# Performance work log

Hardware: AMD Instinct MI355X
Metric: run time of the kernel (lower is better)

## Reference

```python
import jax, jax.numpy as jnp
import numpy as np

NUM_CLASSES = 128
COST_CLS = 2.0
COST_BBOX = 0.25
ALPHA = 0.25
GAMMA = 2.0
BBOX_NORM = np.array([1.0, 1.0, 1.0, 0.1, 0.1, 0.1, 1.0, 1.0, 0.1, 0.1], dtype=np.float32)


def _lsa(cost):
    # Jonker-Volgenant style shortest augmenting path Hungarian (e-maxx formulation).
    # cost: (n, m) float64 with n <= m. Returns col4row: for each row i, assigned column.
    n, m = cost.shape
    INF = 1e18
    a = np.zeros((n + 1, m + 1))
    a[1:, 1:] = cost
    u = np.zeros(n + 1)
    v = np.zeros(m + 1)
    p = np.zeros(m + 1, dtype=np.int64)   # p[j]: row (1-indexed) assigned to col j
    way = np.zeros(m + 1, dtype=np.int64)
    cols = np.arange(1, m + 1)
    for i in range(1, n + 1):
        p[0] = i
        j0 = 0
        minv = np.full(m + 1, INF)
        used = np.zeros(m + 1, dtype=bool)
        while True:
            used[j0] = True
            i0 = p[j0]
            cur = a[i0, 1:] - u[i0] - v[1:]
            better = (~used[1:]) & (cur < minv[1:])
            jb = cols[better]
            minv[jb] = cur[better]
            way[jb] = j0
            free = cols[~used[1:]]
            j1 = free[np.argmin(minv[free])]
            delta = minv[j1]
            uj = np.flatnonzero(used)
            u[p[uj]] += delta
            v[uj] -= delta
            nj = np.flatnonzero(~used)
            minv[nj] -= delta
            j0 = int(j1)
            if p[j0] == 0:
                break
        while j0:
            j1 = way[j0]
            p[j0] = p[j1]
            j0 = j1
    col4row = np.zeros(n, dtype=np.int64)
    for j in range(1, m + 1):
        if p[j]:
            col4row[p[j] - 1] = j - 1
    return col4row


def _match(cls_scores, bbox_preds, gt_labels, gt_bboxes):
    # Matching is done under no_grad in the original; host-side numpy mirrors scipy lsa.
    cs = np.asarray(cls_scores, np.float64)
    bp = np.asarray(bbox_preds, np.float64)
    gl = np.asarray(gt_labels)
    gb = np.asarray(gt_bboxes, np.float64)
    B = cs.shape[0]
    norm = BBOX_NORM.astype(np.float64)
    pred_idx = np.zeros(gl.shape, dtype=np.int64)
    for b in range(B):
        prob = 1.0 / (1.0 + np.exp(-np.clip(cs[b], -20.0, 20.0)))
        cost_cls = -prob[:, gl[b]]                                   # (Q, G)
        pn = np.clip(bp[b] / norm, -100, 100)
        gn = np.clip(gb[b] / norm, -100, 100)
        cost_bbox = np.abs(pn[:, None, :] - gn[None, :, :]).sum(-1)  # (Q, G) L1 cdist
        C = COST_CLS * cost_cls + COST_BBOX * cost_bbox
        pred_idx[b] = _lsa(C.T)   # for each gt g, its matched query index
    return pred_idx


def setup_inputs() -> dict:
    key = jax.random.key(0)
    k1, k2, k3, k4 = jax.random.split(key, 4)
    B, Q, G, C = 64, 2048, 64, NUM_CLASSES
    return {
        "cls_scores": jax.random.normal(k1, (B, Q, C), jnp.float32),
        "bbox_preds": jax.random.normal(k2, (B, Q, 10), jnp.float32),
        "gt_labels": jax.random.randint(k3, (B, G), 0, C),
        "gt_bboxes": jax.random.normal(k4, (B, G, 10), jnp.float32),
    }


def reference(cls_scores, bbox_preds, gt_labels, gt_bboxes):
    pred_idx = jnp.asarray(_match(cls_scores, bbox_preds, gt_labels, gt_bboxes))  # [B, G]
    B, Q, C = cls_scores.shape
    G = gt_labels.shape[1]
    b_idx = jnp.arange(B)[:, None]
    # one-hot classification targets at matched (query, label) positions
    onehot = jnp.zeros((B, Q, C), cls_scores.dtype).at[b_idx, pred_idx, gt_labels].set(1.0)
    prob = jax.nn.sigmoid(cls_scores)
    ce = -(onehot * jax.nn.log_sigmoid(cls_scores)
           + (1.0 - onehot) * jax.nn.log_sigmoid(-cls_scores))
    p_t = prob * onehot + (1.0 - prob) * (1.0 - onehot)
    focal_w = (ALPHA * onehot + (1.0 - ALPHA) * (1.0 - onehot)) * (1.0 - p_t) ** GAMMA
    loss_cls = (ce * focal_w).sum() / (G * B)   # per-batch sum / num_gt, then mean over B
    norm = jnp.asarray(BBOX_NORM)
    mp = bbox_preds[b_idx, pred_idx]            # [B, G, 10] matched predictions
    mg = gt_bboxes                              # gt_indices == arange(G): every gt matched
    loss_bbox = jnp.abs(mp / norm - mg / norm).mean()
    ml = cls_scores[b_idx, pred_idx]
    pos_acc = (jnp.argmax(ml, -1) == gt_labels).astype(jnp.float32).mean()
    xyz_err = jnp.abs(mp[..., :3] - mg[..., :3]).mean()
    matched = jnp.float32(G)
    return jnp.stack([loss_cls, loss_bbox, matched, pos_acc, xyz_err])
```

## Files before the change

### kernel.cpp

```cpp
#include <hip/hip_runtime.h>
#include <math.h>

#define NB 64
#define NQ 2048
#define NG 64
#define NC 128
#define TPB 256

#define WS_NEG   0
#define WS_POS   16384
#define WS_PRED  147456
#define WS_COST  163840
#define WS_NEED  (163840 + (size_t)NB * NG * NQ * 4)

__device__ __forceinline__ float normd(int d) {
    return (d == 3 || d == 4 || d == 5 || d == 8 || d == 9) ? 0.1f : 1.0f;
}
__device__ __forceinline__ float softplus_f(float x) {
    return x > 0.f ? x + log1pf(expf(-x)) : log1pf(expf(x));
}
__device__ __forceinline__ double neg_term(float x) {
    float s = 1.f / (1.f + expf(-x));
    return (double)(0.75f * s * s * softplus_f(x));
}
__device__ __forceinline__ double pos_term(float x) {
    float s = 1.f / (1.f + expf(-x));
    float om = 1.f - s;
    return (double)(0.25f * om * om * softplus_f(-x));
}
__device__ __forceinline__ float neg_term_fast(float x) {
    const float m = fmaxf(x, 0.f);
    const float a = __expf(x - m);
    const float bq = __expf(-m);
    const float den = a + bq;
    const float s = __fdividef(a, den);
    const float sp = m + __logf(den);
    return 0.75f * s * s * sp;
}

__device__ __forceinline__ unsigned dpp_min6(unsigned key) {
    unsigned t;
    t = (unsigned)__builtin_amdgcn_update_dpp((int)key, (int)key, 0x111, 0xF, 0xF, false);
    key = t < key ? t : key;
    t = (unsigned)__builtin_amdgcn_update_dpp((int)key, (int)key, 0x112, 0xF, 0xF, false);
    key = t < key ? t : key;
    t = (unsigned)__builtin_amdgcn_update_dpp((int)key, (int)key, 0x114, 0xF, 0xF, false);
    key = t < key ? t : key;
    t = (unsigned)__builtin_amdgcn_update_dpp((int)key, (int)key, 0x118, 0xF, 0xF, false);
    key = t < key ? t : key;
    t = (unsigned)__builtin_amdgcn_update_dpp((int)key, (int)key, 0x142, 0xF, 0xF, false);
    key = t < key ? t : key;
    t = (unsigned)__builtin_amdgcn_update_dpp((int)key, (int)key, 0x143, 0xF, 0xF, false);
    key = t < key ? t : key;
    return key;
}

__global__ __launch_bounds__(TPB) void cost_neg_kernel(
    const float* __restrict__ cls, const float* __restrict__ bp,
    const int* __restrict__ gl, const float* __restrict__ gb,
    float* __restrict__ C, double* __restrict__ negP)
{
    const int b = blockIdx.x >> 5;
    const int q0 = (blockIdx.x & 31) << 6;
    const int tid = threadIdx.x;
    __shared__ float cls_s[64 * 129];
    __shared__ float pn_s[10 * 64];
    __shared__ float gn_s[64 * 10];
    __shared__ int lbl_s[64];

    double negsum = 0.0;
    const float* clsb = cls + ((size_t)b * NQ + q0) * NC;
    for (int idx = tid; idx < 64 * 128; idx += TPB) {
        const int q = idx >> 7, c = idx & 127;
        const float x = clsb[idx];
        cls_s[q * 129 + c] = x;
        negsum += (double)neg_term_fast(x);
    }
    const float* bpb = bp + ((size_t)b * NQ + q0) * 10;
    for (int idx = tid; idx < 640; idx += TPB) {
        const int q = idx / 10, d = idx % 10;
        const float val = bpb[idx] / normd(d);
        pn_s[d * 64 + q] = fminf(100.f, fmaxf(-100.f, val));
    }
    const float* gbb = gb + (size_t)b * NG * 10;
    for (int idx = tid; idx < 640; idx += TPB) {
        const int g = idx / 10, d = idx % 10;
        const float val = gbb[idx] / normd(d);
        gn_s[g * 10 + d] = fminf(100.f, fmaxf(-100.f, val));
    }
    if (tid < NG) lbl_s[tid] = gl[b * NG + tid];
    __syncthreads();

    const int q = tid & 63;
    float pnq[10];
    #pragma unroll
    for (int d = 0; d < 10; ++d) pnq[d] = pn_s[d * 64 + q];
    for (int g = tid >> 6; g < NG; g += 4) {
        const int lbl = lbl_s[g];
        float x = cls_s[q * 129 + lbl];
        x = fminf(20.f, fmaxf(-20.f, x));
        const float s = __fdividef(1.f, 1.f + __expf(-x));
        float cb = 0.f;
        #pragma unroll
        for (int d = 0; d < 10; ++d) cb += fabsf(pnq[d] - gn_s[g * 10 + d]);
        C[((size_t)(b * NG + g)) * NQ + q0 + q] = -2.f * s + 0.25f * cb;
    }

    #pragma unroll
    for (int off = 32; off; off >>= 1) negsum += __shfl_down(negsum, off);
    __shared__ double bsum[4];
    if ((tid & 63) == 0) bsum[tid >> 6] = negsum;
    __syncthreads();
    if (tid == 0) negP[blockIdx.x] = bsum[0] + bsum[1] + bsum[2] + bsum[3];
}

__global__ __launch_bounds__(64, 1) void hungarian5_kernel(
    const float* __restrict__ C, int* __restrict__ pred)
{
    const int b = blockIdx.x;
    const int lane = threadIdx.x;
    __shared__ float u[NG + 1];
    __shared__ float usedD[NQ + 1];
    __shared__ int p[NQ + 1];
    __shared__ int way32[NQ + 1];

    for (int j = lane; j <= NQ; j += 64) { p[j] = 0; way32[j] = 0; }
    if (lane <= NG) u[lane] = 0.f;
    __syncthreads();

    const float* Cb = C + (size_t)b * NG * NQ;
    const int qbase = lane << 5;

    float vv[32];
    #pragma unroll
    for (int k = 0; k < 32; ++k) vv[k] = -16.f;
    unsigned amask = 0;

    float4 nx[8];
    {
        const float* r0 = Cb + qbase;
        #pragma unroll
        for (int m = 0; m < 8; ++m) nx[m] = reinterpret_cast<const float4*>(r0)[m];
    }

    for (int i = 1; i <= NG; ++i) {
        float madj[32];
        unsigned um = 0;

        unsigned m0 = 0xFFFFFFFFu, m1 = 0xFFFFFFFFu, m2 = 0xFFFFFFFFu, m3 = 0xFFFFFFFFu;
        #pragma unroll
        for (int m = 0; m < 8; ++m) {
            const float d0 = nx[m].x - vv[4*m+0];
            const float d1 = nx[m].y - vv[4*m+1];
            const float d2 = nx[m].z - vv[4*m+2];
            const float d3 = nx[m].w - vv[4*m+3];
            madj[4*m+0] = d0; madj[4*m+1] = d1; madj[4*m+2] = d2; madj[4*m+3] = d3;
            const unsigned k0 = (__float_as_uint(d0) & 0xFFFFF800u) | (unsigned)(qbase + 4*m+0);
            const unsigned k1 = (__float_as_uint(d1) & 0xFFFFF800u) | (unsigned)(qbase + 4*m+1);
            const unsigned k2 = (__float_as_uint(d2) & 0xFFFFF800u) | (unsigned)(qbase + 4*m+2);
            const unsigned k3 = (__float_as_uint(d3) & 0xFFFFF800u) | (unsigned)(qbase + 4*m+3);
            m0 = k0 < m0 ? k0 : m0;  m1 = k1 < m1 ? k1 : m1;
            m2 = k2 < m2 ? k2 : m2;  m3 = k3 < m3 ? k3 : m3;
        }
        if (i < NG) {
            const float* rn = Cb + (size_t)i * NQ + qbase;
            #pragma unroll
            for (int m = 0; m < 8; ++m) nx[m] = reinterpret_cast<const float4*>(rn)[m];
        }
        const unsigned ma = m0 < m1 ? m0 : m1;
        const unsigned mb = m2 < m3 ? m2 : m3;
        unsigned gkey = (unsigned)__builtin_amdgcn_readlane(
                            (int)dpp_min6(ma < mb ? ma : mb), 63);
        int q1 = (int)(gkey & 2047u);
        float D = __uint_as_float(gkey & 0xFFFFF800u);
        int ow = q1 >> 5, kk = q1 & 31;
        unsigned am_ow = (unsigned)__builtin_amdgcn_readlane((int)amask, ow);
        const bool assigned0 = (am_ow >> kk) & 1u;

        if (!assigned0) {
            if (lane == 0) { u[i] += D; p[q1 + 1] = i; }
        } else {
            if (lane == ow) { um |= 1u << kk; usedD[q1 + 1] = D; }
            #pragma unroll
            for (int k = 0; k < 32; ++k)
                if (k == kk && lane == ow) madj[k] = 1e30f;
            int j0 = q1 + 1;
            int i0 = p[j0];
            while (true) {
                const float s = u[i0] - D;
                const float* rr = Cb + (size_t)(i0 - 1) * NQ + qbase;
                float4 t[8];
                #pragma unroll
                for (int m = 0; m < 8; ++m) t[m] = reinterpret_cast<const float4*>(rr)[m];
                unsigned bk = 0xFFFFFFFFu;
                #pragma unroll
                for (int m = 0; m < 8; ++m) {
                    const float c[4] = {t[m].x, t[m].y, t[m].z, t[m].w};
                    #pragma unroll
                    for (int d = 0; d < 4; ++d) {
                        const int k = 4*m + d;
                        const float cand = c[d] - vv[k] - s;
                        if (!((um >> k) & 1u) && cand < madj[k]) {
                            madj[k] = cand;
                            way32[qbase + k + 1] = (i << 16) | j0;
                        }
                        const unsigned kb = (__float_as_uint(madj[k]) & 0xFFFFF800u)
                                          | (unsigned)(qbase + k);
                        bk = kb < bk ? kb : bk;
                    }
                }
                gkey = (unsigned)__builtin_amdgcn_readlane((int)dpp_min6(bk), 63);
                q1 = (int)(gkey & 2047u);
                D = __uint_as_float(gkey & 0xFFFFF800u);
                ow = q1 >> 5; kk = q1 & 31;
                am_ow = (unsigned)__builtin_amdgcn_readlane((int)amask, ow);
                if (!((am_ow >> kk) & 1u)) break;
                if (lane == ow) { um |= 1u << kk; usedD[q1 + 1] = D; }
                #pragma unroll
                for (int k = 0; k < 32; ++k)
                    if (k == kk && lane == ow) madj[k] = 1e30f;
                j0 = q1 + 1;
                i0 = p[j0];
            }
            #pragma unroll
            for (int k = 0; k < 32; ++k) {
                if ((um >> k) & 1u) {
                    const int j = qbase + k + 1;
                    const float dd = D - usedD[j];
                    vv[k] -= dd;
                    u[p[j]] += dd;
                }
            }
            if (lane == 0) {
                u[i] += D;
                int j = q1 + 1;
                while (true) {
                    const int w = way32[j];
                    const int par = ((w >> 16) == i) ? (w & 0xFFFF) : 0;
                    p[j] = par ? p[par] : i;
                    if (!par) break;
                    j = par;
                }
            }
        }
        if (lane == ow) amask |= 1u << kk;
    }

    for (int j = lane + 1; j <= NQ; j += 64) {
        const int pi = p[j];
        if (pi > 0) pred[b * NG + pi - 1] = j - 1;
    }
}

__global__ __launch_bounds__(TPB) void hungarian_fb_kernel(
    const float* __restrict__ cls, const float* __restrict__ bp,
    const int* __restrict__ gl, const float* __restrict__ gb,
    int* __restrict__ pred)
{
    const int b = blockIdx.x;
    const int tid = threadIdx.x;
    __shared__ float pn[10][NQ];
    __shared__ float gn[NG][10];
    __shared__ int lbls[NG];
    __shared__ double u[NG + 1];
    __shared__ double v[NQ + 1];
    __shared__ double minv[NQ + 1];
    __shared__ int p[NQ + 1];
    __shared__ int way[NQ + 1];
    __shared__ unsigned char used[NQ + 4];
    __shared__ double red_v[4];
    __shared__ int red_j[4];
    __shared__ int s_j0;
    __shared__ double s_delta;

    const float* bpb = bp + (size_t)b * NQ * 10;
    for (int idx = tid; idx < NQ * 10; idx += TPB) {
        int q = idx / 10, d = idx % 10;
        float val = bpb[idx] / normd(d);
        pn[d][q] = fminf(100.f, fmaxf(-100.f, val));
    }
    const float* gbb = gb + (size_t)b * NG * 10;
    for (int idx = tid; idx < NG * 10; idx += TPB) {
        int g = idx / 10, d = idx % 10;
        float val = gbb[idx] / normd(d);
        gn[g][d] = fminf(100.f, fmaxf(-100.f, val));
    }
    if (tid < NG) lbls[tid] = gl[b * NG + tid];
    for (int j = tid; j <= NQ; j += TPB) { v[j] = 0.0; p[j] = 0; way[j] = 0; }
    if (tid <= NG) u[tid] = 0.0;
    __syncthreads();

    const float* clsb = cls + (size_t)b * NQ * NC;

    for (int i = 1; i <= NG; ++i) {
        for (int j = tid; j <= NQ; j += TPB) { minv[j] = 1e18; used[j] = 0; }
        if (tid == 0) { p[0] = i; s_j0 = 0; }
        __syncthreads();
        while (true) {
            const int j0 = s_j0;
            if (tid == 0) used[j0] = 1;
            __syncthreads();
            const int i0 = p[j0];
            const int g = i0 - 1;
            const int lbl = lbls[g];
            const double ui0 = u[i0];
            double bestv = 1e30; int bestj = NQ + 1;
            for (int j = tid + 1; j <= NQ; j += TPB) {
                if (!used[j]) {
                    const int q = j - 1;
                    float x = clsb[(size_t)q * NC + lbl];
                    x = fminf(20.f, fmaxf(-20.f, x));
                    const double prob = 1.0 / (1.0 + exp((double)(-x)));
                    float cb = 0.f;
                    #pragma unroll
                    for (int d = 0; d < 10; ++d) cb += fabsf(pn[d][q] - gn[g][d]);
                    const double cur = -2.0 * prob + 0.25 * (double)cb - ui0 - v[j];
                    if (cur < minv[j]) { minv[j] = cur; way[j] = j0; }
                    const double mv = minv[j];
                    if (mv < bestv) { bestv = mv; bestj = j; }
                }
            }
            #pragma unroll
            for (int off = 32; off; off >>= 1) {
                const double ov = __shfl_down(bestv, off);
                const int oj = __shfl_down(bestj, off);
                if (ov < bestv || (ov == bestv && oj < bestj)) { bestv = ov; bestj = oj; }
            }
            if ((tid & 63) == 0) { red_v[tid >> 6] = bestv; red_j[tid >> 6] = bestj; }
            __syncthreads();
            if (tid == 0) {
                for (int w = 1; w < 4; ++w)
                    if (red_v[w] < bestv || (red_v[w] == bestv && red_j[w] < bestj)) {
                        bestv = red_v[w]; bestj = red_j[w];
                    }
                s_delta = bestv; s_j0 = bestj;
            }
            __syncthreads();
            const double delta = s_delta;
            const int j1 = s_j0;
            for (int j = tid; j <= NQ; j += TPB) {
                if (used[j]) { u[p[j]] += delta; v[j] -= delta; }
                else minv[j] -= delta;
            }
            __syncthreads();
            if (p[j1] == 0) break;
        }
        if (tid == 0) {
            int j = s_j0;
            while (j) { const int jn = way[j]; p[j] = p[jn]; j = jn; }
        }
        __syncthreads();
    }

    for (int j = tid + 1; j <= NQ; j += TPB) {
        const int pi = p[j];
        if (pi > 0) pred[b * NG + pi - 1] = j - 1;
    }
}

__global__ __launch_bounds__(TPB) void neg_fb_kernel(const float* __restrict__ cls,
                                                     double* __restrict__ negP, long n4) {
    const long stride = (long)gridDim.x * blockDim.x;
    double sum = 0.0;
    for (long i = (long)blockIdx.x * blockDim.x + threadIdx.x; i < n4; i += stride) {
        const float4 xv = reinterpret_cast<const float4*>(cls)[i];
        sum += (double)neg_term_fast(xv.x) + (double)neg_term_fast(xv.y)
             + (double)neg_term_fast(xv.z) + (double)neg_term_fast(xv.w);
    }
    #pragma unroll
    for (int off = 32; off; off >>= 1) sum += __shfl_down(sum, off);
    __shared__ double bsum[4];
    if ((threadIdx.x & 63) == 0) bsum[threadIdx.x >> 6] = sum;
    __syncthreads();
    if (threadIdx.x == 0) negP[blockIdx.x] = bsum[0] + bsum[1] + bsum[2] + bsum[3];
}

__global__ __launch_bounds__(TPB) void pos_kernel(
    const float* __restrict__ cls, const float* __restrict__ bp,
    const int* __restrict__ gl, const float* __restrict__ gb,
    const int* __restrict__ pred, double* __restrict__ posP)
{
    const int wid = (int)((blockIdx.x * blockDim.x + threadIdx.x) >> 6);
    const int lane = threadIdx.x & 63;
    if (wid >= NB * NG) return;
    const int b = wid >> 6;
    const int pq = pred[wid];
    const int lbl = gl[wid];
    const float* row = cls + ((size_t)b * NQ + pq) * NC;
    const float v1 = row[lane];
    const float v2 = row[lane + 64];
    float bv; int bi;
    if (v2 > v1) { bv = v2; bi = lane + 64; } else { bv = v1; bi = lane; }
    #pragma unroll
    for (int off = 32; off; off >>= 1) {
        const float ov = __shfl_down(bv, off);
        const int oi = __shfl_down(bi, off);
        if (ov > bv || (ov == bv && oi < bi)) { bv = ov; bi = oi; }
    }
    const float xl = __shfl(v1, lbl & 63);
    const float xh = __shfl(v2, lbl & 63);
    const float x = (lbl < 64) ? xl : xh;
    double bterm = 0.0, xterm = 0.0;
    if (lane < 10) {
        const float mp = bp[((size_t)b * NQ + pq) * 10 + lane];
        const float mg = gb[(size_t)wid * 10 + lane];
        const float nr = normd(lane);
        bterm = (double)fabsf(mp / nr - mg / nr);
        if (lane < 3) xterm = (double)fabsf(mp - mg);
    }
    #pragma unroll
    for (int off = 8; off; off >>= 1) {
        bterm += __shfl_down(bterm, off);
        xterm += __shfl_down(xterm, off);
    }
    if (lane == 0) {
        double* e = posP + (size_t)wid * 4;
        e[0] = pos_term(x) - neg_term(x);
        e[1] = bterm;
        e[2] = (bi == lbl) ? 1.0 : 0.0;
        e[3] = xterm;
    }
}

__global__ __launch_bounds__(TPB) void final_kernel(const double* __restrict__ ws,
                                                    float* __restrict__ out) {
    const int tid = threadIdx.x;
    const double* negP = ws;
    const double* posP = ws + 2048;
    double s[5] = {0, 0, 0, 0, 0};
    for (int i = tid; i < 2048; i += TPB) s[0] += negP[i];
    for (int i = tid; i < 4096; i += TPB) {
        const double* e = posP + (size_t)i * 4;
        s[1] += e[0]; s[2] += e[1]; s[3] += e[2]; s[4] += e[3];
    }
    __shared__ double red[4][5];
    #pragma unroll
    for (int c = 0; c < 5; ++c) {
        #pragma unroll
        for (int off = 32; off; off >>= 1) s[c] += __shfl_down(s[c], off);
    }
    if ((tid & 63) == 0) {
        #pragma unroll
        for (int c = 0; c < 5; ++c) red[tid >> 6][c] = s[c];
    }
    __syncthreads();
    if (tid == 0) {
        #pragma unroll
        for (int c = 0; c < 5; ++c) s[c] = red[0][c] + red[1][c] + red[2][c] + red[3][c];
        out[0] = (float)((s[0] + s[1]) / 4096.0);
        out[1] = (float)(s[2] / 40960.0);
        out[2] = 64.0f;
        out[3] = (float)(s[3] / 4096.0);
        out[4] = (float)(s[4] / 12288.0);
    }
}

extern "C" void kernel_launch(void* const* d_in, const int* in_sizes, int n_in,
                              void* d_out, int out_size, void* d_ws, size_t ws_size,
                              hipStream_t stream) {
    const float* cls = (const float*)d_in[0];
    const float* bp  = (const float*)d_in[1];
    const int*   gl  = (const int*)d_in[2];
    const float* gb  = (const float*)d_in[3];
    float* out = (float*)d_out;
    double* negP = (double*)((char*)d_ws + WS_NEG);
    double* posP = (double*)((char*)d_ws + WS_POS);
    int* pred    = (int*)((char*)d_ws + WS_PRED);
    float* C     = (float*)((char*)d_ws + WS_COST);

    if (ws_size >= WS_NEED) {
        hipLaunchKernelGGL(cost_neg_kernel, dim3(NB * 32), dim3(TPB), 0, stream,
                           cls, bp, gl, gb, C, negP);
        hipLaunchKernelGGL(hungarian5_kernel, dim3(NB), dim3(64), 0, stream, C, pred);
    } else {
        hipLaunchKernelGGL(hungarian_fb_kernel, dim3(NB), dim3(TPB), 0, stream,
                           cls, bp, gl, gb, pred);
        const long n4 = (long)NB * NQ * NC / 4;
        hipLaunchKernelGGL(neg_fb_kernel, dim3(2048), dim3(TPB), 0, stream, cls, negP, n4);
    }
    hipLaunchKernelGGL(pos_kernel, dim3((NB * NG * 64) / TPB), dim3(TPB), 0, stream,
                       cls, bp, gl, gb, pred, posP);
    hipLaunchKernelGGL(final_kernel, dim3(1), dim3(TPB), 0, stream, (double*)d_ws, out);
}
```

Baseline: 215.2 us.

## Store cost matrix in fp16 and double-buffer row prefetch in Hungarian kernel

The cost matrix written by the cost kernel is stored as fp16 instead of fp32, halving the global memory traffic that the serial Hungarian solver reads on every augmenting step. The Hungarian loop is restructured into a per-row helper with two register buffers, so each row's prefetch runs two rows ahead. The cost kernel's class-score load is also vectorised to float4. Reduced precision can change tie-breaking and the resulting assignments, although the key already truncates the low mantissa bits.

New measurement: 189.3 us. 1.14x faster.

```diff
diff --git a/kernel.cpp b/kernel.cpp
--- a/kernel.cpp
+++ b/kernel.cpp
@@ -1,4 +1,5 @@
 #include <hip/hip_runtime.h>
+#include <hip/hip_fp16.h>
 #include <math.h>
 
 #define NB 64
@@ -11,7 +12,7 @@
 #define WS_POS   16384
 #define WS_PRED  147456
 #define WS_COST  163840
-#define WS_NEED  (163840 + (size_t)NB * NG * NQ * 4)
+#define WS_NEED  (163840 + (size_t)NB * NG * NQ * 2)
 
 __device__ __forceinline__ float normd(int d) {
     return (d == 3 || d == 4 || d == 5 || d == 8 || d == 9) ? 0.1f : 1.0f;
@@ -58,7 +59,7 @@
 __global__ __launch_bounds__(TPB) void cost_neg_kernel(
     const float* __restrict__ cls, const float* __restrict__ bp,
     const int* __restrict__ gl, const float* __restrict__ gb,
-    float* __restrict__ C, double* __restrict__ negP)
+    unsigned short* __restrict__ Ch, double* __restrict__ negP)
 {
     const int b = blockIdx.x >> 5;
     const int q0 = (blockIdx.x & 31) << 6;
@@ -70,11 +71,17 @@
 
     double negsum = 0.0;
     const float* clsb = cls + ((size_t)b * NQ + q0) * NC;
-    for (int idx = tid; idx < 64 * 128; idx += TPB) {
-        const int q = idx >> 7, c = idx & 127;
-        const float x = clsb[idx];
-        cls_s[q * 129 + c] = x;
-        negsum += (double)neg_term_fast(x);
+    const float4* cls4 = reinterpret_cast<const float4*>(clsb);
+    #pragma unroll
+    for (int it = 0; it < 8; ++it) {
+        const int idx4 = it * TPB + tid;
+        const float4 xv = cls4[idx4];
+        const int e0 = idx4 << 2;
+        float* dst = &cls_s[(e0 >> 7) * 129 + (e0 & 127)];
+        dst[0] = xv.x; dst[1] = xv.y; dst[2] = xv.z; dst[3] = xv.w;
+        const float s4 = neg_term_fast(xv.x) + neg_term_fast(xv.y)
+                       + neg_term_fast(xv.z) + neg_term_fast(xv.w);
+        negsum += (double)s4;
     }
     const float* bpb = bp + ((size_t)b * NQ + q0) * 10;
     for (int idx = tid; idx < 640; idx += TPB) {
@@ -103,7 +110,9 @@
         float cb = 0.f;
         #pragma unroll
         for (int d = 0; d < 10; ++d) cb += fabsf(pnq[d] - gn_s[g * 10 + d]);
-        C[((size_t)(b * NG + g)) * NQ + q0 + q] = -2.f * s + 0.25f * cb;
+        const float cost = -2.f * s + 0.25f * cb;
+        Ch[((size_t)(b * NG + g)) * NQ + q0 + q] =
+            __builtin_bit_cast(unsigned short, __float2half_rn(cost));
     }
 
     #pragma unroll
@@ -114,8 +123,125 @@
     if (tid == 0) negP[blockIdx.x] = bsum[0] + bsum[1] + bsum[2] + bsum[3];
 }
 
-__global__ __launch_bounds__(64, 1) void hungarian5_kernel(
-    const float* __restrict__ C, int* __restrict__ pred)
+__device__ __forceinline__ void jv_row(
+    const int i, uint4 (&buf)[4], const unsigned short* __restrict__ Cb16,
+    float (&vv)[32], unsigned& amask, const int lane, const int qbase,
+    float* u, float* usedD, int* p, int* way32)
+{
+    float cf[32];
+    #pragma unroll
+    for (int m = 0; m < 4; ++m) {
+        const unsigned arr[4] = {buf[m].x, buf[m].y, buf[m].z, buf[m].w};
+        #pragma unroll
+        for (int d = 0; d < 4; ++d) {
+            const __half2 h = __builtin_bit_cast(__half2, arr[d]);
+            cf[m * 8 + d * 2]     = __low2float(h);
+            cf[m * 8 + d * 2 + 1] = __high2float(h);
+        }
+    }
+    float madj[32];
+    unsigned m0 = 0xFFFFFFFFu, m1 = 0xFFFFFFFFu, m2 = 0xFFFFFFFFu, m3 = 0xFFFFFFFFu;
+    #pragma unroll
+    for (int k = 0; k < 32; ++k) {
+        const float cand = cf[k] - vv[k];
+        madj[k] = cand;
+        const unsigned kb = (__float_as_uint(cand) & 0xFFFFF800u) | (unsigned)(qbase + k);
+        if ((k & 3) == 0)      m0 = kb < m0 ? kb : m0;
+        else if ((k & 3) == 1) m1 = kb < m1 ? kb : m1;
+        else if ((k & 3) == 2) m2 = kb < m2 ? kb : m2;
+        else                   m3 = kb < m3 ? kb : m3;
+    }
+    if (i + 2 <= NG) {
+        const uint4* rp = reinterpret_cast<const uint4*>(
+                              Cb16 + (size_t)(i + 1) * NQ) + lane * 4;
+        buf[0] = rp[0]; buf[1] = rp[1]; buf[2] = rp[2]; buf[3] = rp[3];
+    }
+    const unsigned ma = m0 < m1 ? m0 : m1;
+    const unsigned mb = m2 < m3 ? m2 : m3;
+    unsigned gkey = (unsigned)__builtin_amdgcn_readlane(
+                        (int)dpp_min6(ma < mb ? ma : mb), 63);
+    int q1 = (int)(gkey & 2047u);
+    float D = __uint_as_float(gkey & 0xFFFFF800u);
+    int ow = q1 >> 5, kk = q1 & 31;
+    unsigned am_ow = (unsigned)__builtin_amdgcn_readlane((int)amask, ow);
+
+    if (!((am_ow >> kk) & 1u)) {
+        if (lane == 0) { u[i] += D; p[q1 + 1] = i; }
+    } else {
+        unsigned um = 0;
+        if (lane == ow) { um |= 1u << kk; usedD[q1 + 1] = D; }
+        #pragma unroll
+        for (int k = 0; k < 32; ++k)
+            if (k == kk && lane == ow) madj[k] = 1e30f;
+        int j0 = q1 + 1;
+        int i0 = p[j0];
+        while (true) {
+            const float s = u[i0] - D;
+            const uint4* rp = reinterpret_cast<const uint4*>(
+                                  Cb16 + (size_t)(i0 - 1) * NQ) + lane * 4;
+            const uint4 t[4] = {rp[0], rp[1], rp[2], rp[3]};
+            float tc[32];
+            #pragma unroll
+            for (int m = 0; m < 4; ++m) {
+                const unsigned arr[4] = {t[m].x, t[m].y, t[m].z, t[m].w};
+                #pragma unroll
+                for (int d = 0; d < 4; ++d) {
+                    const __half2 h = __builtin_bit_cast(__half2, arr[d]);
+                    tc[m * 8 + d * 2]     = __low2float(h);
+                    tc[m * 8 + d * 2 + 1] = __high2float(h);
+                }
+            }
+            unsigned bk = 0xFFFFFFFFu;
+            #pragma unroll
+            for (int k = 0; k < 32; ++k) {
+                const float cand = tc[k] - vv[k] - s;
+                if (!((um >> k) & 1u) && cand < madj[k]) {
+                    madj[k] = cand;
+                    way32[qbase + k + 1] = (i << 16) | j0;
+                }
+                const unsigned kb = (__float_as_uint(madj[k]) & 0xFFFFF800u)
+                                  | (unsigned)(qbase + k);
+                bk = kb < bk ? kb : bk;
+            }
+            gkey = (unsigned)__builtin_amdgcn_readlane((int)dpp_min6(bk), 63);
+            q1 = (int)(gkey & 2047u);
+            D = __uint_as_float(gkey & 0xFFFFF800u);
+            ow = q1 >> 5; kk = q1 & 31;
+            am_ow = (unsigned)__builtin_amdgcn_readlane((int)amask, ow);
+            if (!((am_ow >> kk) & 1u)) break;
+            if (lane == ow) { um |= 1u << kk; usedD[q1 + 1] = D; }
+            #pragma unroll
+            for (int k = 0; k < 32; ++k)
+                if (k == kk && lane == ow) madj[k] = 1e30f;
+            j0 = q1 + 1;
+            i0 = p[j0];
+        }
+        #pragma unroll
+        for (int k = 0; k < 32; ++k) {
+            if ((um >> k) & 1u) {
+                const int j = qbase + k + 1;
+                const float dd = D - usedD[j];
+                vv[k] -= dd;
+                u[p[j]] += dd;
+            }
+        }
+        if (lane == 0) {
+            u[i] += D;
+            int j = q1 + 1;
+            while (true) {
+                const int w = way32[j];
+                const int par = ((w >> 16) == i) ? (w & 0xFFFF) : 0;
+                p[j] = par ? p[par] : i;
+                if (!par) break;
+                j = par;
+            }
+        }
+    }
+    if (lane == ow) amask |= 1u << kk;
+}
+
+__global__ __launch_bounds__(64, 1) void hungarian6_kernel(
+    const unsigned short* __restrict__ Ch, int* __restrict__ pred)
 {
     const int b = blockIdx.x;
     const int lane = threadIdx.x;
@@ -128,7 +254,7 @@
     if (lane <= NG) u[lane] = 0.f;
     __syncthreads();
 
-    const float* Cb = C + (size_t)b * NG * NQ;
+    const unsigned short* Cb16 = Ch + (size_t)b * NG * NQ;
     const int qbase = lane << 5;
 
     float vv[32];
@@ -136,114 +262,17 @@
     for (int k = 0; k < 32; ++k) vv[k] = -16.f;
     unsigned amask = 0;
 
-    float4 nx[8];
+    uint4 A[4], B[4];
     {
-        const float* r0 = Cb + qbase;
-        #pragma unroll
-        for (int m = 0; m < 8; ++m) nx[m] = reinterpret_cast<const float4*>(r0)[m];
-    }
-
-    for (int i = 1; i <= NG; ++i) {
-        float madj[32];
-        unsigned um = 0;
-
-        unsigned m0 = 0xFFFFFFFFu, m1 = 0xFFFFFFFFu, m2 = 0xFFFFFFFFu, m3 = 0xFFFFFFFFu;
-        #pragma unroll
-        for (int m = 0; m < 8; ++m) {
-            const float d0 = nx[m].x - vv[4*m+0];
-            const float d1 = nx[m].y - vv[4*m+1];
-            const float d2 = nx[m].z - vv[4*m+2];
-            const float d3 = nx[m].w - vv[4*m+3];
-            madj[4*m+0] = d0; madj[4*m+1] = d1; madj[4*m+2] = d2; madj[4*m+3] = d3;
-            const unsigned k0 = (__float_as_uint(d0) & 0xFFFFF800u) | (unsigned)(qbase + 4*m+0);
-            const unsigned k1 = (__float_as_uint(d1) & 0xFFFFF800u) | (unsigned)(qbase + 4*m+1);
-            const unsigned k2 = (__float_as_uint(d2) & 0xFFFFF800u) | (unsigned)(qbase + 4*m+2);
-            const unsigned k3 = (__float_as_uint(d3) & 0xFFFFF800u) | (unsigned)(qbase + 4*m+3);
-            m0 = k0 < m0 ? k0 : m0;  m1 = k1 < m1 ? k1 : m1;
-            m2 = k2 < m2 ? k2 : m2;  m3 = k3 < m3 ? k3 : m3;
-        }
-        if (i < NG) {
-            const float* rn = Cb + (size_t)i * NQ + qbase;
-            #pragma unroll
-            for (int m = 0; m < 8; ++m) nx[m] = reinterpret_cast<const float4*>(rn)[m];
-        }
-        const unsigned ma = m0 < m1 ? m0 : m1;
-        const unsigned mb = m2 < m3 ? m2 : m3;
-        unsigned gkey = (unsigned)__builtin_amdgcn_readlane(
-                            (int)dpp_min6(ma < mb ? ma : mb), 63);
-        int q1 = (int)(gkey & 2047u);
-        float D = __uint_as_float(gkey & 0xFFFFF800u);
-        int ow = q1 >> 5, kk = q1 & 31;
-        unsigned am_ow = (unsigned)__builtin_amdgcn_readlane((int)amask, ow);
-        const bool assigned0 = (am_ow >> kk) & 1u;
-
-        if (!assigned0) {
-            if (lane == 0) { u[i] += D; p[q1 + 1] = i; }
-        } else {
-            if (lane == ow) { um |= 1u << kk; usedD[q1 + 1] = D; }
-            #pragma unroll
-            for (int k = 0; k < 32; ++k)
-                if (k == kk && lane == ow) madj[k] = 1e30f;
-            int j0 = q1 + 1;
-            int i0 = p[j0];
-            while (true) {
-                const float s = u[i0] - D;
-                const float* rr = Cb + (size_t)(i0 - 1) * NQ + qbase;
-                float4 t[8];
-                #pragma unroll
-                for (int m = 0; m < 8; ++m) t[m] = reinterpret_cast<const float4*>(rr)[m];
-                unsigned bk = 0xFFFFFFFFu;
-                #pragma unroll
-                for (int m = 0; m < 8; ++m) {
-                    const float c[4] = {t[m].x, t[m].y, t[m].z, t[m].w};
-                    #pragma unroll
-                    for (int d = 0; d < 4; ++d) {
-                        const int k = 4*m + d;
-                        const float cand = c[d] - vv[k] - s;
-                        if (!((um >> k) & 1u) && cand < madj[k]) {
-                            madj[k] = cand;
-                            way32[qbase + k + 1] = (i << 16) | j0;
-                        }
-                        const unsigned kb = (__float_as_uint(madj[k]) & 0xFFFFF800u)
-                                          | (unsigned)(qbase + k);
-                        bk = kb < bk ? kb : bk;
-                    }
-                }
-                gkey = (unsigned)__builtin_amdgcn_readlane((int)dpp_min6(bk), 63);
-                q1 = (int)(gkey & 2047u);
-                D = __uint_as_float(gkey & 0xFFFFF800u);
-                ow = q1 >> 5; kk = q1 & 31;
-                am_ow = (unsigned)__builtin_amdgcn_readlane((int)amask, ow);
-                if (!((am_ow >> kk) & 1u)) break;
-                if (lane == ow) { um |= 1u << kk; usedD[q1 + 1] = D; }
-                #pragma unroll
-                for (int k = 0; k < 32; ++k)
-                    if (k == kk && lane == ow) madj[k] = 1e30f;
-                j0 = q1 + 1;
-                i0 = p[j0];
-            }
-            #pragma unroll
-            for (int k = 0; k < 32; ++k) {
-                if ((um >> k) & 1u) {
-                    const int j = qbase + k + 1;
-                    const float dd = D - usedD[j];
-                    vv[k] -= dd;
-                    u[p[j]] += dd;
-                }
-            }
-            if (lane == 0) {
-                u[i] += D;
-                int j = q1 + 1;
-                while (true) {
-                    const int w = way32[j];
-                    const int par = ((w >> 16) == i) ? (w & 0xFFFF) : 0;
-                    p[j] = par ? p[par] : i;
-                    if (!par) break;
-                    j = par;
-                }
-            }
-        }
-        if (lane == ow) amask |= 1u << kk;
+        const uint4* r0 = reinterpret_cast<const uint4*>(Cb16) + lane * 4;
+        const uint4* r1 = reinterpret_cast<const uint4*>(Cb16 + NQ) + lane * 4;
+        A[0] = r0[0]; A[1] = r0[1]; A[2] = r0[2]; A[3] = r0[3];
+        B[0] = r1[0]; B[1] = r1[1]; B[2] = r1[2]; B[3] = r1[3];
+    }
+
+    for (int i = 1; i <= NG; i += 2) {
+        jv_row(i,     A, Cb16, vv, amask, lane, qbase, u, usedD, p, way32);
+        jv_row(i + 1, B, Cb16, vv, amask, lane, qbase, u, usedD, p, way32);
     }
 
     for (int j = lane + 1; j <= NQ; j += 64) {
@@ -466,12 +495,12 @@
     double* negP = (double*)((char*)d_ws + WS_NEG);
     double* posP = (double*)((char*)d_ws + WS_POS);
     int* pred    = (int*)((char*)d_ws + WS_PRED);
-    float* C     = (float*)((char*)d_ws + WS_COST);
+    unsigned short* Ch = (unsigned short*)((char*)d_ws + WS_COST);
 
     if (ws_size >= WS_NEED) {
         hipLaunchKernelGGL(cost_neg_kernel, dim3(NB * 32), dim3(TPB), 0, stream,
-                           cls, bp, gl, gb, C, negP);
-        hipLaunchKernelGGL(hungarian5_kernel, dim3(NB), dim3(64), 0, stream, C, pred);
+                           cls, bp, gl, gb, Ch, negP);
+        hipLaunchKernelGGL(hungarian6_kernel, dim3(NB), dim3(64), 0, stream, Ch, pred);
     } else {
         hipLaunchKernelGGL(hungarian_fb_kernel, dim3(NB), dim3(TPB), 0, stream,
                            cls, bp, gl, gb, pred);
```
